# Kernel optimization log

Hardware: AMD Instinct MI355X
Metric: run time of the kernel (lower is better)

## Reference

```python
import jax, jax.numpy as jnp
import numpy as np


def setup_inputs() -> dict:
    key = jax.random.key(0)
    k1, k2, k3 = jax.random.split(key, 3)
    B, C, H, W = 64, 2048, 14, 14
    M, NC = 32, 396
    x = jax.random.normal(k1, (B, C, H, W), dtype=jnp.float32)
    Wa = jax.random.normal(k2, (M, C), dtype=jnp.float32) * (1.0 / np.sqrt(C))
    ba = jnp.zeros((M,), dtype=jnp.float32)
    Wc = jax.random.normal(k3, (NC, M * C), dtype=jnp.float32) * (1.0 / np.sqrt(M * C))
    bc = jnp.zeros((NC,), dtype=jnp.float32)
    return {"x": x, "Wa": Wa, "ba": ba, "Wc": Wc, "bc": bc}


def reference(x, Wa, ba, Wc, bc):
    # x: [B, C, H, W]
    B, C, H, W = x.shape
    M = Wa.shape[0]
    # 1x1 conv == channel contraction; attention maps [B, M, H, W]
    A = jax.nn.sigmoid(jnp.einsum('bchw,mc->bmhw', x, Wa) + ba[None, :, None, None])
    # BAP: per-head attention-weighted global average pool -> [B, M, C]
    bap = jnp.einsum('bchw,bmhw->bmc', x, A) / (H * W)
    feats = bap.reshape(B, M * C)  # concat head-major, matching torch cat order
    return feats @ Wc.T + bc
```

## Files before the change

### kernel.cpp

```cpp
#include <hip/hip_runtime.h>
#include <hip/hip_bf16.h>
#include <cstdint>

#define B_N 64
#define C_N 2048
#define HW_N 196
#define HWP 224
#define M_N 32
#define NC_N 396
#define K_N 65536
#define CCH 256
#define NCH 8
#define ZSTRIDE (B_N * M_N * HW_N)

typedef __attribute__((ext_vector_type(8))) short bf16x8;
typedef __attribute__((ext_vector_type(4))) float f32x4;

__device__ inline short f2bf(float x) {
  union { float f; unsigned u; } v; v.f = x;
  unsigned r = (v.u + 0x7FFFu + ((v.u >> 16) & 1u)) >> 16;
  return (short)r;
}

__device__ inline unsigned packbf2(float lo, float hi) {
  return ((unsigned)(unsigned short)f2bf(hi) << 16) |
         (unsigned)(unsigned short)f2bf(lo);
}

__global__ __launch_bounds__(256) void k1a_partial(
    const float* __restrict__ x, const float* __restrict__ Wa,
    float* __restrict__ z) {
  __shared__ short waT[32][264];
  __shared__ short xT[208][40];
  const int t = threadIdx.x;
  const int w = t >> 6, lane = t & 63, lq = lane >> 4, ln = lane & 15;
  const int cx = blockIdx.x, b = blockIdx.y;
  const int c0 = cx * CCH;

  unsigned* xTw = (unsigned*)xT;
  if (t < 240) xTw[196 * 20 + t] = 0u;
  for (int i = t; i < 2048; i += 256) {
    int m = i >> 6, f4 = i & 63;
    float4 v = *(const float4*)(Wa + (size_t)m * C_N + c0 + f4 * 4);
    uint2 pk;
    pk.x = packbf2(v.x, v.y);
    pk.y = packbf2(v.z, v.w);
    *(uint2*)((char*)waT + m * 528 + f4 * 8) = pk;
  }

  f32x4 acc[4][2];
#pragma unroll
  for (int ti = 0; ti < 4; ++ti) {
    acc[ti][0] = (f32x4){0.f, 0.f, 0.f, 0.f};
    acc[ti][1] = (f32x4){0.f, 0.f, 0.f, 0.f};
  }

  const float* __restrict__ xb0 = x + (size_t)b * (C_N * HW_N) + (size_t)c0 * HW_N;
  const int p0 = t & 15;
  const int q0 = t >> 4;

  for (int ss = 0; ss < 8; ++ss) {
    const float* xs = xb0 + (size_t)ss * 32 * HW_N;
    {
      const float* r0 = xs + (2 * p0) * HW_N + 4 * q0;
      float4 fa0 = *(const float4*)r0;
      float4 fb0 = *(const float4*)(r0 + HW_N);
      float4 fa1 = *(const float4*)(r0 + 64);
      float4 fb1 = *(const float4*)(r0 + 64 + HW_N);
      float4 fa2 = *(const float4*)(r0 + 128);
      float4 fb2 = *(const float4*)(r0 + 128 + HW_N);
      unsigned* d0 = xTw + q0 * 80 + p0;
      d0[0]  = packbf2(fa0.x, fb0.x);
      d0[20] = packbf2(fa0.y, fb0.y);
      d0[40] = packbf2(fa0.z, fb0.z);
      d0[60] = packbf2(fa0.w, fb0.w);
      unsigned* d1 = d0 + 1280;
      d1[0]  = packbf2(fa1.x, fb1.x);
      d1[20] = packbf2(fa1.y, fb1.y);
      d1[40] = packbf2(fa1.z, fb1.z);
      d1[60] = packbf2(fa1.w, fb1.w);
      unsigned* d2 = d0 + 2560;
      d2[0]  = packbf2(fa2.x, fb2.x);
      d2[20] = packbf2(fa2.y, fb2.y);
      d2[40] = packbf2(fa2.z, fb2.z);
      d2[60] = packbf2(fa2.w, fb2.w);
      if (t < 16) {
        const float* r3 = xs + (2 * t) * HW_N + 192;
        float4 fa3 = *(const float4*)r3;
        float4 fb3 = *(const float4*)(r3 + HW_N);
        unsigned* d3 = xTw + 48 * 80 + t;
        d3[0]  = packbf2(fa3.x, fb3.x);
        d3[20] = packbf2(fa3.y, fb3.y);
        d3[40] = packbf2(fa3.z, fb3.z);
        d3[60] = packbf2(fa3.w, fb3.w);
      }
    }
    __syncthreads();
    const int kb = ss * 64 + lq * 16;
    bf16x8 af0 = *(const bf16x8*)((const char*)waT + ln * 528 + kb);
    bf16x8 af1 = *(const bf16x8*)((const char*)waT + (16 + ln) * 528 + kb);
#pragma unroll
    for (int ti = 0; ti < 4; ++ti) {
      int ht = w + ti * 4;
      if (ht < 13) {
        bf16x8 bfr = *(const bf16x8*)((const char*)xT + (ht * 16 + ln) * 80 + lq * 16);
        acc[ti][0] = __builtin_amdgcn_mfma_f32_16x16x32_bf16(af0, bfr, acc[ti][0], 0, 0, 0);
        acc[ti][1] = __builtin_amdgcn_mfma_f32_16x16x32_bf16(af1, bfr, acc[ti][1], 0, 0, 0);
      }
    }
    __syncthreads();
  }

  float* zc = z + (size_t)(cx * B_N + b) * (M_N * HW_N);
#pragma unroll
  for (int ti = 0; ti < 4; ++ti) {
    int ht = w + ti * 4;
    if (ht < 13) {
      int hw = ht * 16 + ln;
      if (hw < HW_N) {
#pragma unroll
        for (int mt = 0; mt < 2; ++mt) {
#pragma unroll
          for (int r = 0; r < 4; ++r) {
            int m = mt * 16 + lq * 4 + r;
            zc[(size_t)m * HW_N + hw] = acc[ti][mt][r];
          }
        }
      }
    }
  }
}

__global__ __launch_bounds__(256) void k1b_sig(
    const float* __restrict__ z, const float* __restrict__ ba,
    short* __restrict__ Apad) {
  int idx = blockIdx.x * 256 + threadIdx.x;
  int b = idx / (M_N * HWP);
  int r = idx - b * (M_N * HWP);
  int m = r / HWP;
  int hw = r - m * HWP;
  short out = 0;
  if (hw < HW_N) {
    float s = ba[m];
    size_t base = ((size_t)b * M_N + m) * HW_N + hw;
#pragma unroll
    for (int cx = 0; cx < NCH; ++cx)
      s += z[(size_t)cx * ZSTRIDE + base];
    out = f2bf(1.f / (1.f + __expf(-s)));
  }
  Apad[idx] = out;
}

__global__ __launch_bounds__(256) void k2_bap(
    const float* __restrict__ x, const short* __restrict__ Apad,
    short* __restrict__ featsb) {
  const int t = threadIdx.x;
  const int w = t >> 6, lane = t & 63, lq = lane >> 4, ln = lane & 15;
  const int b = blockIdx.y;
  const int c = blockIdx.x * 64 + w * 16 + ln;
  const float* __restrict__ xrow = x + (size_t)b * (C_N * HW_N) + (size_t)c * HW_N;
  const short* __restrict__ ap0 = Apad + ((size_t)b * M_N + ln) * HWP + lq * 8;
  const short* __restrict__ ap1 = ap0 + 16 * HWP;

  f32x4 d0 = {0.f, 0.f, 0.f, 0.f}, d1 = {0.f, 0.f, 0.f, 0.f};
#pragma unroll
  for (int s = 0; s < 7; ++s) {
    bf16x8 a0 = *(const bf16x8*)(ap0 + s * 32);
    bf16x8 a1 = *(const bf16x8*)(ap1 + s * 32);
    bf16x8 bfr;
    const int h = s * 32 + lq * 8;
    if (s < 6) {
      float4 b0 = *(const float4*)(xrow + h);
      float4 b1 = *(const float4*)(xrow + h + 4);
      bfr[0]=f2bf(b0.x); bfr[1]=f2bf(b0.y); bfr[2]=f2bf(b0.z); bfr[3]=f2bf(b0.w);
      bfr[4]=f2bf(b1.x); bfr[5]=f2bf(b1.y); bfr[6]=f2bf(b1.z); bfr[7]=f2bf(b1.w);
    } else {
      float4 b0 = make_float4(0.f, 0.f, 0.f, 0.f);
      if (lq == 0) b0 = *(const float4*)(xrow + h);
      bfr[0]=f2bf(b0.x); bfr[1]=f2bf(b0.y); bfr[2]=f2bf(b0.z); bfr[3]=f2bf(b0.w);
      bfr[4]=0; bfr[5]=0; bfr[6]=0; bfr[7]=0;
    }
    d0 = __builtin_amdgcn_mfma_f32_16x16x32_bf16(a0, bfr, d0, 0, 0, 0);
    d1 = __builtin_amdgcn_mfma_f32_16x16x32_bf16(a1, bfr, d1, 0, 0, 0);
  }
  const float sc = 1.f / (float)HW_N;
  const int bt = b >> 4, bl = b & 15;
  const int lq2 = (c >> 3) & 3, j = c & 7;
  const int cs5 = c >> 5;
  short* fb = featsb + ((size_t)bt * 64 + (size_t)lq2 * 16 + bl) * 8 + j;
#pragma unroll
  for (int r = 0; r < 4; ++r) {
    int m0 = lq * 4 + r;
    fb[(size_t)(m0 * 64 + cs5) * 2048]        = f2bf(d0[r] * sc);
    fb[(size_t)((16 + m0) * 64 + cs5) * 2048] = f2bf(d1[r] * sc);
  }
}

__global__ __launch_bounds__(256) void k3_cls(
    const short* __restrict__ featsb, const float* __restrict__ Wc,
    float* __restrict__ partial) {
  const int t = threadIdx.x;
  const int w = t >> 6, lane = t & 63, lq = lane >> 4, ln = lane & 15;
  const int n = blockIdx.x * 64 + w * 16 + ln;
  const int nc = n < NC_N ? n : NC_N - 1;
  const int kc = blockIdx.y;
  const size_t k0 = (size_t)kc * 512;
  const float* __restrict__ wrow = Wc + (size_t)nc * K_N + k0 + lq * 8;
  const short* __restrict__ fb = featsb + (size_t)(kc * 16) * 2048 + lane * 8;

  f32x4 acc0 = {0.f,0.f,0.f,0.f}, acc1 = {0.f,0.f,0.f,0.f};
  f32x4 acc2 = {0.f,0.f,0.f,0.f}, acc3 = {0.f,0.f,0.f,0.f};

  float4 cw0 = *(const float4*)(wrow);
  float4 cw1 = *(const float4*)(wrow + 4);
  bf16x8 ca0 = *(const bf16x8*)(fb);
  bf16x8 ca1 = *(const bf16x8*)(fb + 512);
  bf16x8 ca2 = *(const bf16x8*)(fb + 1024);
  bf16x8 ca3 = *(const bf16x8*)(fb + 1536);

#pragma unroll
  for (int s = 0; s < 16; ++s) {
    float4 nw0, nw1; bf16x8 na0, na1, na2, na3;
    if (s < 15) {
      const float* wn = wrow + (s + 1) * 32;
      nw0 = *(const float4*)(wn);
      nw1 = *(const float4*)(wn + 4);
      const short* fs = fb + (size_t)(s + 1) * 2048;
      na0 = *(const bf16x8*)(fs);
      na1 = *(const bf16x8*)(fs + 512);
      na2 = *(const bf16x8*)(fs + 1024);
      na3 = *(const bf16x8*)(fs + 1536);
    }
    bf16x8 bfr;
    bfr[0]=f2bf(cw0.x); bfr[1]=f2bf(cw0.y); bfr[2]=f2bf(cw0.z); bfr[3]=f2bf(cw0.w);
    bfr[4]=f2bf(cw1.x); bfr[5]=f2bf(cw1.y); bfr[6]=f2bf(cw1.z); bfr[7]=f2bf(cw1.w);
    acc0 = __builtin_amdgcn_mfma_f32_16x16x32_bf16(ca0, bfr, acc0, 0, 0, 0);
    acc1 = __builtin_amdgcn_mfma_f32_16x16x32_bf16(ca1, bfr, acc1, 0, 0, 0);
    acc2 = __builtin_amdgcn_mfma_f32_16x16x32_bf16(ca2, bfr, acc2, 0, 0, 0);
    acc3 = __builtin_amdgcn_mfma_f32_16x16x32_bf16(ca3, bfr, acc3, 0, 0, 0);
    if (s < 15) {
      cw0 = nw0; cw1 = nw1;
      ca0 = na0; ca1 = na1; ca2 = na2; ca3 = na3;
    }
  }
  if (n < NC_N) {
    float* po = partial + (size_t)blockIdx.y * (B_N * NC_N) + n;
#pragma unroll
    for (int r = 0; r < 4; ++r) {
      int br = lq * 4 + r;
      po[(size_t)br * NC_N]        = acc0[r];
      po[(size_t)(16 + br) * NC_N] = acc1[r];
      po[(size_t)(32 + br) * NC_N] = acc2[r];
      po[(size_t)(48 + br) * NC_N] = acc3[r];
    }
  }
}

__global__ __launch_bounds__(256) void k4_reduce(
    const float* __restrict__ partial, const float* __restrict__ bc,
    float* __restrict__ out) {
  int idx = blockIdx.x * 256 + threadIdx.x;
  if (idx >= B_N * NC_N) return;
  int n = idx % NC_N;
  float s = bc[n];
#pragma unroll 8
  for (int kc = 0; kc < 128; ++kc) s += partial[(size_t)kc * (B_N * NC_N) + idx];
  out[idx] = s;
}

extern "C" void kernel_launch(void* const* d_in, const int* in_sizes, int n_in,
                              void* d_out, int out_size, void* d_ws, size_t ws_size,
                              hipStream_t stream) {
  const float* x  = (const float*)d_in[0];
  const float* Wa = (const float*)d_in[1];
  const float* ba = (const float*)d_in[2];
  const float* Wc = (const float*)d_in[3];
  const float* bc = (const float*)d_in[4];
  float* out = (float*)d_out;

  char* wsb = (char*)d_ws;
  short* Apad    = (short*)(wsb);
  short* featsb  = (short*)(wsb + (1u  << 20));
  float* partial = (float*)(wsb + (10u << 20));
  float* zbuf    = (float*)(wsb + (10u << 20));
  (void)ws_size; (void)in_sizes; (void)n_in; (void)out_size;

  hipLaunchKernelGGL(k1a_partial, dim3(NCH, B_N), dim3(256), 0, stream,
                     x, Wa, zbuf);
  hipLaunchKernelGGL(k1b_sig, dim3(1792), dim3(256), 0, stream,
                     zbuf, ba, Apad);
  hipLaunchKernelGGL(k2_bap, dim3(32, 64), dim3(256), 0, stream,
                     x, Apad, featsb);
  hipLaunchKernelGGL(k3_cls, dim3(7, 128), dim3(256), 0, stream,
                     featsb, Wc, partial);
  hipLaunchKernelGGL(k4_reduce, dim3(99), dim3(256), 0, stream,
                     partial, bc, out);
}
```

Baseline: 279.4 us.

## Double-buffer k1a, stage k2 output through LDS, halve k3 K-split

k1a gets a double-buffered LDS tile, so the global loads for the next channel slab overlap the MFMAs on the current one, and one barrier per iteration is removed. k2 now handles four batches per block and writes its bf16 features into shared memory, then stores them to global as coalesced 16-byte vectors instead of scattered 2-byte writes. k3 doubles the K chunk per block (64 chunks instead of 128), which halves the partial buffer that k4 has to reduce. The costs are more registers and LDS in k1a and k2, and fewer blocks in k2 and k3, which lowers parallelism.

```diff
diff --git a/kernel.cpp b/kernel.cpp
--- a/kernel.cpp
+++ b/kernel.cpp
@@ -11,6 +11,7 @@
 #define K_N 65536
 #define CCH 256
 #define NCH 8
+#define KCH 64
 #define ZSTRIDE (B_N * M_N * HW_N)
 
 typedef __attribute__((ext_vector_type(8))) short bf16x8;
@@ -31,14 +32,15 @@
     const float* __restrict__ x, const float* __restrict__ Wa,
     float* __restrict__ z) {
   __shared__ short waT[32][264];
-  __shared__ short xT[208][40];
+  __shared__ short xT[2][208][40];
   const int t = threadIdx.x;
   const int w = t >> 6, lane = t & 63, lq = lane >> 4, ln = lane & 15;
   const int cx = blockIdx.x, b = blockIdx.y;
   const int c0 = cx * CCH;
 
-  unsigned* xTw = (unsigned*)xT;
-  if (t < 240) xTw[196 * 20 + t] = 0u;
+  unsigned* xTw0 = (unsigned*)xT[0];
+  unsigned* xTw1 = (unsigned*)xT[1];
+  if (t < 240) { xTw0[196 * 20 + t] = 0u; xTw1[196 * 20 + t] = 0u; }
   for (int i = t; i < 2048; i += 256) {
     int m = i >> 6, f4 = i & 63;
     float4 v = *(const float4*)(Wa + (size_t)m * C_N + c0 + f4 * 4);
@@ -59,43 +61,54 @@
   const int p0 = t & 15;
   const int q0 = t >> 4;
 
+  float4 fa0, fb0, fa1, fb1, fa2, fb2, fa3, fb3;
+  auto LD = [&](int ss) {
+    const float* xs = xb0 + (size_t)ss * 32 * HW_N;
+    const float* r0 = xs + (2 * p0) * HW_N + 4 * q0;
+    fa0 = *(const float4*)r0;
+    fb0 = *(const float4*)(r0 + HW_N);
+    fa1 = *(const float4*)(r0 + 64);
+    fb1 = *(const float4*)(r0 + 64 + HW_N);
+    fa2 = *(const float4*)(r0 + 128);
+    fb2 = *(const float4*)(r0 + 128 + HW_N);
+    if (t < 16) {
+      const float* r3 = xs + (2 * t) * HW_N + 192;
+      fa3 = *(const float4*)r3;
+      fb3 = *(const float4*)(r3 + HW_N);
+    }
+  };
+  auto STORE = [&](unsigned* xw) {
+    unsigned* d0 = xw + q0 * 80 + p0;
+    d0[0]  = packbf2(fa0.x, fb0.x);
+    d0[20] = packbf2(fa0.y, fb0.y);
+    d0[40] = packbf2(fa0.z, fb0.z);
+    d0[60] = packbf2(fa0.w, fb0.w);
+    unsigned* d1 = d0 + 1280;
+    d1[0]  = packbf2(fa1.x, fb1.x);
+    d1[20] = packbf2(fa1.y, fb1.y);
+    d1[40] = packbf2(fa1.z, fb1.z);
+    d1[60] = packbf2(fa1.w, fb1.w);
+    unsigned* d2 = d0 + 2560;
+    d2[0]  = packbf2(fa2.x, fb2.x);
+    d2[20] = packbf2(fa2.y, fb2.y);
+    d2[40] = packbf2(fa2.z, fb2.z);
+    d2[60] = packbf2(fa2.w, fb2.w);
+    if (t < 16) {
+      unsigned* d3 = xw + 48 * 80 + t;
+      d3[0]  = packbf2(fa3.x, fb3.x);
+      d3[20] = packbf2(fa3.y, fb3.y);
+      d3[40] = packbf2(fa3.z, fb3.z);
+      d3[60] = packbf2(fa3.w, fb3.w);
+    }
+  };
+
+  LD(0);
+  STORE(xTw0);
+  __syncthreads();
+
   for (int ss = 0; ss < 8; ++ss) {
-    const float* xs = xb0 + (size_t)ss * 32 * HW_N;
-    {
-      const float* r0 = xs + (2 * p0) * HW_N + 4 * q0;
-      float4 fa0 = *(const float4*)r0;
-      float4 fb0 = *(const float4*)(r0 + HW_N);
-      float4 fa1 = *(const float4*)(r0 + 64);
-      float4 fb1 = *(const float4*)(r0 + 64 + HW_N);
-      float4 fa2 = *(const float4*)(r0 + 128);
-      float4 fb2 = *(const float4*)(r0 + 128 + HW_N);
-      unsigned* d0 = xTw + q0 * 80 + p0;
-      d0[0]  = packbf2(fa0.x, fb0.x);
-      d0[20] = packbf2(fa0.y, fb0.y);
-      d0[40] = packbf2(fa0.z, fb0.z);
-      d0[60] = packbf2(fa0.w, fb0.w);
-      unsigned* d1 = d0 + 1280;
-      d1[0]  = packbf2(fa1.x, fb1.x);
-      d1[20] = packbf2(fa1.y, fb1.y);
-      d1[40] = packbf2(fa1.z, fb1.z);
-      d1[60] = packbf2(fa1.w, fb1.w);
-      unsigned* d2 = d0 + 2560;
-      d2[0]  = packbf2(fa2.x, fb2.x);
-      d2[20] = packbf2(fa2.y, fb2.y);
-      d2[40] = packbf2(fa2.z, fb2.z);
-      d2[60] = packbf2(fa2.w, fb2.w);
-      if (t < 16) {
-        const float* r3 = xs + (2 * t) * HW_N + 192;
-        float4 fa3 = *(const float4*)r3;
-        float4 fb3 = *(const float4*)(r3 + HW_N);
-        unsigned* d3 = xTw + 48 * 80 + t;
-        d3[0]  = packbf2(fa3.x, fb3.x);
-        d3[20] = packbf2(fa3.y, fb3.y);
-        d3[40] = packbf2(fa3.z, fb3.z);
-        d3[60] = packbf2(fa3.w, fb3.w);
-      }
-    }
-    __syncthreads();
+    if (ss < 7) LD(ss + 1);
+    const char* xb = (const char*)xT[ss & 1];
     const int kb = ss * 64 + lq * 16;
     bf16x8 af0 = *(const bf16x8*)((const char*)waT + ln * 528 + kb);
     bf16x8 af1 = *(const bf16x8*)((const char*)waT + (16 + ln) * 528 + kb);
@@ -103,11 +116,12 @@
     for (int ti = 0; ti < 4; ++ti) {
       int ht = w + ti * 4;
       if (ht < 13) {
-        bf16x8 bfr = *(const bf16x8*)((const char*)xT + (ht * 16 + ln) * 80 + lq * 16);
+        bf16x8 bfr = *(const bf16x8*)(xb + (ht * 16 + ln) * 80 + lq * 16);
         acc[ti][0] = __builtin_amdgcn_mfma_f32_16x16x32_bf16(af0, bfr, acc[ti][0], 0, 0, 0);
         acc[ti][1] = __builtin_amdgcn_mfma_f32_16x16x32_bf16(af1, bfr, acc[ti][1], 0, 0, 0);
       }
     }
+    if (ss < 7) STORE((ss & 1) ? xTw0 : xTw1);
     __syncthreads();
   }
 
@@ -154,46 +168,66 @@
 __global__ __launch_bounds__(256) void k2_bap(
     const float* __restrict__ x, const short* __restrict__ Apad,
     short* __restrict__ featsb) {
+  __shared__ short tb[8192];
   const int t = threadIdx.x;
   const int w = t >> 6, lane = t & 63, lq = lane >> 4, ln = lane & 15;
-  const int b = blockIdx.y;
-  const int c = blockIdx.x * 64 + w * 16 + ln;
-  const float* __restrict__ xrow = x + (size_t)b * (C_N * HW_N) + (size_t)c * HW_N;
-  const short* __restrict__ ap0 = Apad + ((size_t)b * M_N + ln) * HWP + lq * 8;
-  const short* __restrict__ ap1 = ap0 + 16 * HWP;
-
-  f32x4 d0 = {0.f, 0.f, 0.f, 0.f}, d1 = {0.f, 0.f, 0.f, 0.f};
-#pragma unroll
-  for (int s = 0; s < 7; ++s) {
-    bf16x8 a0 = *(const bf16x8*)(ap0 + s * 32);
-    bf16x8 a1 = *(const bf16x8*)(ap1 + s * 32);
-    bf16x8 bfr;
-    const int h = s * 32 + lq * 8;
-    if (s < 6) {
-      float4 b0 = *(const float4*)(xrow + h);
-      float4 b1 = *(const float4*)(xrow + h + 4);
-      bfr[0]=f2bf(b0.x); bfr[1]=f2bf(b0.y); bfr[2]=f2bf(b0.z); bfr[3]=f2bf(b0.w);
-      bfr[4]=f2bf(b1.x); bfr[5]=f2bf(b1.y); bfr[6]=f2bf(b1.z); bfr[7]=f2bf(b1.w);
-    } else {
-      float4 b0 = make_float4(0.f, 0.f, 0.f, 0.f);
-      if (lq == 0) b0 = *(const float4*)(xrow + h);
-      bfr[0]=f2bf(b0.x); bfr[1]=f2bf(b0.y); bfr[2]=f2bf(b0.z); bfr[3]=f2bf(b0.w);
-      bfr[4]=0; bfr[5]=0; bfr[6]=0; bfr[7]=0;
-    }
-    d0 = __builtin_amdgcn_mfma_f32_16x16x32_bf16(a0, bfr, d0, 0, 0, 0);
-    d1 = __builtin_amdgcn_mfma_f32_16x16x32_bf16(a1, bfr, d1, 0, 0, 0);
-  }
+  const int cx = blockIdx.x;
+  const int bq = blockIdx.y;
+  const int cl = w * 16 + ln;
+  const int c = cx * 64 + cl;
   const float sc = 1.f / (float)HW_N;
-  const int bt = b >> 4, bl = b & 15;
-  const int lq2 = (c >> 3) & 3, j = c & 7;
-  const int cs5 = c >> 5;
-  short* fb = featsb + ((size_t)bt * 64 + (size_t)lq2 * 16 + bl) * 8 + j;
-#pragma unroll
-  for (int r = 0; r < 4; ++r) {
-    int m0 = lq * 4 + r;
-    fb[(size_t)(m0 * 64 + cs5) * 2048]        = f2bf(d0[r] * sc);
-    fb[(size_t)((16 + m0) * 64 + cs5) * 2048] = f2bf(d1[r] * sc);
-  }
+  const int och = cl >> 5, lq2w = (cl >> 3) & 3, j = cl & 7;
+
+#pragma unroll
+  for (int bi = 0; bi < 4; ++bi) {
+    const int b = bq * 4 + bi;
+    const float* __restrict__ xrow = x + (size_t)b * (C_N * HW_N) + (size_t)c * HW_N;
+    const short* __restrict__ ap0 = Apad + ((size_t)b * M_N + ln) * HWP + lq * 8;
+    const short* __restrict__ ap1 = ap0 + 16 * HWP;
+
+    f32x4 d0 = {0.f, 0.f, 0.f, 0.f}, d1 = {0.f, 0.f, 0.f, 0.f};
+#pragma unroll
+    for (int s = 0; s < 7; ++s) {
+      bf16x8 a0 = *(const bf16x8*)(ap0 + s * 32);
+      bf16x8 a1 = *(const bf16x8*)(ap1 + s * 32);
+      bf16x8 bfr;
+      const int h = s * 32 + lq * 8;
+      if (s < 6) {
+        float4 b0 = *(const float4*)(xrow + h);
+        float4 b1 = *(const float4*)(xrow + h + 4);
+        bfr[0]=f2bf(b0.x); bfr[1]=f2bf(b0.y); bfr[2]=f2bf(b0.z); bfr[3]=f2bf(b0.w);
+        bfr[4]=f2bf(b1.x); bfr[5]=f2bf(b1.y); bfr[6]=f2bf(b1.z); bfr[7]=f2bf(b1.w);
+      } else {
+        float4 b0 = make_float4(0.f, 0.f, 0.f, 0.f);
+        if (lq == 0) b0 = *(const float4*)(xrow + h);
+        bfr[0]=f2bf(b0.x); bfr[1]=f2bf(b0.y); bfr[2]=f2bf(b0.z); bfr[3]=f2bf(b0.w);
+        bfr[4]=0; bfr[5]=0; bfr[6]=0; bfr[7]=0;
+      }
+      d0 = __builtin_amdgcn_mfma_f32_16x16x32_bf16(a0, bfr, d0, 0, 0, 0);
+      d1 = __builtin_amdgcn_mfma_f32_16x16x32_bf16(a1, bfr, d1, 0, 0, 0);
+    }
+#pragma unroll
+    for (int r = 0; r < 4; ++r) {
+      int m0 = lq * 4 + r;
+      tb[m0 * 256 + och * 128 + lq2w * 32 + bi * 8 + j]        = f2bf(d0[r] * sc);
+      tb[(16 + m0) * 256 + och * 128 + lq2w * 32 + bi * 8 + j] = f2bf(d1[r] * sc);
+    }
+  }
+  __syncthreads();
+
+  const int me = t >> 3, oche = (t >> 2) & 1, lq2e = t & 3;
+  const short* srcp = tb + t * 32;
+  uint4 v0 = *(const uint4*)(srcp);
+  uint4 v1 = *(const uint4*)(srcp + 8);
+  uint4 v2 = *(const uint4*)(srcp + 16);
+  uint4 v3 = *(const uint4*)(srcp + 24);
+  const int sg = me * 64 + cx * 2 + oche;
+  const int bt = bq >> 2;
+  short* dst = featsb + (size_t)(sg * 4 + bt) * 512 + lq2e * 128 + (bq & 3) * 32;
+  *(uint4*)(dst)      = v0;
+  *(uint4*)(dst + 8)  = v1;
+  *(uint4*)(dst + 16) = v2;
+  *(uint4*)(dst + 24) = v3;
 }
 
 __global__ __launch_bounds__(256) void k3_cls(
@@ -204,9 +238,9 @@
   const int n = blockIdx.x * 64 + w * 16 + ln;
   const int nc = n < NC_N ? n : NC_N - 1;
   const int kc = blockIdx.y;
-  const size_t k0 = (size_t)kc * 512;
+  const size_t k0 = (size_t)kc * 1024;
   const float* __restrict__ wrow = Wc + (size_t)nc * K_N + k0 + lq * 8;
-  const short* __restrict__ fb = featsb + (size_t)(kc * 16) * 2048 + lane * 8;
+  const short* __restrict__ fb = featsb + (size_t)(kc * 32) * 2048 + lane * 8;
 
   f32x4 acc0 = {0.f,0.f,0.f,0.f}, acc1 = {0.f,0.f,0.f,0.f};
   f32x4 acc2 = {0.f,0.f,0.f,0.f}, acc3 = {0.f,0.f,0.f,0.f};
@@ -219,9 +253,9 @@
   bf16x8 ca3 = *(const bf16x8*)(fb + 1536);
 
 #pragma unroll
-  for (int s = 0; s < 16; ++s) {
+  for (int s = 0; s < 32; ++s) {
     float4 nw0, nw1; bf16x8 na0, na1, na2, na3;
-    if (s < 15) {
+    if (s < 31) {
       const float* wn = wrow + (s + 1) * 32;
       nw0 = *(const float4*)(wn);
       nw1 = *(const float4*)(wn + 4);
@@ -238,13 +272,13 @@
     acc1 = __builtin_amdgcn_mfma_f32_16x16x32_bf16(ca1, bfr, acc1, 0, 0, 0);
     acc2 = __builtin_amdgcn_mfma_f32_16x16x32_bf16(ca2, bfr, acc2, 0, 0, 0);
     acc3 = __builtin_amdgcn_mfma_f32_16x16x32_bf16(ca3, bfr, acc3, 0, 0, 0);
-    if (s < 15) {
+    if (s < 31) {
       cw0 = nw0; cw1 = nw1;
       ca0 = na0; ca1 = na1; ca2 = na2; ca3 = na3;
     }
   }
   if (n < NC_N) {
-    float* po = partial + (size_t)blockIdx.y * (B_N * NC_N) + n;
+    float* po = partial + (size_t)kc * (B_N * NC_N) + n;
 #pragma unroll
     for (int r = 0; r < 4; ++r) {
       int br = lq * 4 + r;
@@ -264,7 +298,7 @@
   int n = idx % NC_N;
   float s = bc[n];
 #pragma unroll 8
-  for (int kc = 0; kc < 128; ++kc) s += partial[(size_t)kc * (B_N * NC_N) + idx];
+  for (int kc = 0; kc < KCH; ++kc) s += partial[(size_t)kc * (B_N * NC_N) + idx];
   out[idx] = s;
 }
 
@@ -289,9 +323,9 @@
                      x, Wa, zbuf);
   hipLaunchKernelGGL(k1b_sig, dim3(1792), dim3(256), 0, stream,
                      zbuf, ba, Apad);
-  hipLaunchKernelGGL(k2_bap, dim3(32, 64), dim3(256), 0, stream,
+  hipLaunchKernelGGL(k2_bap, dim3(32, 16), dim3(256), 0, stream,
                      x, Apad, featsb);
-  hipLaunchKernelGGL(k3_cls, dim3(7, 128), dim3(256), 0, stream,
+  hipLaunchKernelGGL(k3_cls, dim3(7, KCH), dim3(256), 0, stream,
                      featsb, Wc, partial);
   hipLaunchKernelGGL(k4_reduce, dim3(99), dim3(256), 0, stream,
                      partial, bc, out);
```

Measured after the change: 270.5 us. 1.03x faster.
